# Performance work log

Measured on AMD Instinct MI355X. Metric: run time of the kernel, lower is better.

The kernel has to match this reference:

```python
import jax, jax.numpy as jnp
import numpy as np

NUM_HEADS = 16
NUM_KV_HEADS = 4
HEAD_DIM = 128
DIM = 2048
B, S = 2, 2048


def apply_rotary(t, cos, sin):
    # t: [B, S, H, D]; cos/sin: [S, D//2] -> broadcast [1, S, 1, D//2]
    tr = t.reshape(*t.shape[:-1], HEAD_DIM // 2, 2)
    t_r, t_i = tr[..., 0], tr[..., 1]
    c = cos[None, :, None, :]
    s = sin[None, :, None, :]
    o_r = t_r * c - t_i * s
    o_i = t_r * s + t_i * c
    return jnp.stack([o_r, o_i], axis=-1).reshape(t.shape)


def setup_inputs() -> dict:
    key = jax.random.key(0)
    ks = jax.random.split(key, 7)
    sc = 1.0 / np.sqrt(DIM)
    x = jax.random.normal(ks[0], (B, S, DIM), jnp.float32)
    pos = jnp.arange(S, dtype=jnp.float32)[:, None]
    inv_freq = 1.0 / (10000.0 ** (jnp.arange(0, HEAD_DIM, 2, dtype=jnp.float32) / HEAD_DIM))
    ang = pos * inv_freq[None, :]
    freqs_cos = jnp.cos(ang)
    freqs_sin = jnp.sin(ang)
    w_q = jax.random.normal(ks[1], (DIM, NUM_HEADS * HEAD_DIM), jnp.float32) * sc
    w_k = jax.random.normal(ks[2], (DIM, NUM_KV_HEADS * HEAD_DIM), jnp.float32) * sc
    w_v = jax.random.normal(ks[3], (DIM, NUM_KV_HEADS * HEAD_DIM), jnp.float32) * sc
    w_o = jax.random.normal(ks[4], (NUM_HEADS * HEAD_DIM, DIM), jnp.float32) * sc
    return {"x": x, "freqs_cos": freqs_cos, "freqs_sin": freqs_sin,
            "w_q": w_q, "w_k": w_k, "w_v": w_v, "w_o": w_o}


def reference(x, freqs_cos, freqs_sin, w_q, w_k, w_v, w_o):
    b, s, _ = x.shape
    kv_rep = NUM_HEADS // NUM_KV_HEADS
    q = (x @ w_q).reshape(b, s, NUM_HEADS, HEAD_DIM)
    k = (x @ w_k).reshape(b, s, NUM_KV_HEADS, HEAD_DIM)
    v = (x @ w_v).reshape(b, s, NUM_KV_HEADS, HEAD_DIM)
    q = apply_rotary(q, freqs_cos, freqs_sin)
    k = apply_rotary(k, freqs_cos, freqs_sin)
    # GQA: repeat KV heads to match query heads
    k = jnp.repeat(k, kv_rep, axis=2)
    v = jnp.repeat(v, kv_rep, axis=2)
    scores = jnp.einsum('bqhd,bkhd->bhqk', q, k) / np.sqrt(HEAD_DIM)
    causal = jnp.triu(jnp.full((s, s), -jnp.inf, jnp.float32), k=1)
    scores = scores + causal[None, None, :, :]
    attn = jax.nn.softmax(scores, axis=-1)
    out = jnp.einsum('bhqk,bkhd->bqhd', attn, v).reshape(b, s, NUM_HEADS * HEAD_DIM)
    return out @ w_o
```

## Files before the change

kernel.cpp:

```cpp
#include <hip/hip_runtime.h>
#include <stdint.h>

#define DIMSZ 2048
#define NH 16
#define NKV 4
#define HD 128
#define BATCH 2
#define SEQ 2048
#define MROWS (BATCH*SEQ)
#define NQKV (NH*HD + 2*NKV*HD)

typedef unsigned short u16;
typedef float f32x4 __attribute__((ext_vector_type(4)));
typedef short short8 __attribute__((ext_vector_type(8)));
typedef __bf16 bf16x8 __attribute__((ext_vector_type(8)));
typedef unsigned short u16x4 __attribute__((ext_vector_type(4)));

__device__ __forceinline__ u16 f2bf(float f) {
  __bf16 h = (__bf16)f;
  return __builtin_bit_cast(u16, h);
}

__device__ __forceinline__ float bf2f(u16 h) {
  union { uint32_t u; float f; } v; v.u = ((uint32_t)h) << 16; return v.f;
}

__device__ __forceinline__ void async16(void* lds, const void* g) {
  __builtin_amdgcn_global_load_lds(
      (const __attribute__((address_space(1))) void*)(g),
      (__attribute__((address_space(3))) void*)(lds), 16, 0, 0);
}

__device__ __forceinline__ bf16x8 load_frag(const u16* p) {
  short8 v = *reinterpret_cast<const short8*>(p);
  return __builtin_bit_cast(bf16x8, v);
}

__global__ void cast_x_kernel(const float* __restrict__ x, u16* __restrict__ xb) {
  int i = (blockIdx.x * blockDim.x + threadIdx.x) * 4;
  float4 v = *reinterpret_cast<const float4*>(x + i);
  u16x4 o;
  o.x = f2bf(v.x); o.y = f2bf(v.y); o.z = f2bf(v.z); o.w = f2bf(v.w);
  *reinterpret_cast<u16x4*>(xb + i) = o;
}

__global__ __launch_bounds__(1024) void wtrans_all_kernel(const float* __restrict__ wq,
                                                          const float* __restrict__ wk,
                                                          const float* __restrict__ wv,
                                                          const float* __restrict__ wo,
                                                          u16* __restrict__ wtqkv,
                                                          u16* __restrict__ wto) {
  __shared__ float t[32][33];
  int y = blockIdx.y;
  const float* src; int srcN; u16* dst; int nbase;
  if (y < 64)      { src = wq; srcN = 2048; dst = wtqkv;                          nbase = y * 32; }
  else if (y < 80) { src = wk; srcN = 512;  dst = wtqkv + (size_t)2048 * 2048;    nbase = (y - 64) * 32; }
  else if (y < 96) { src = wv; srcN = 512;  dst = wtqkv + (size_t)2560 * 2048;    nbase = (y - 80) * 32; }
  else             { src = wo; srcN = 2048; dst = wto;                            nbase = (y - 96) * 32; }
  int k0 = blockIdx.x * 32;
  int tx = threadIdx.x, ty = threadIdx.y;
  t[ty][tx] = src[(size_t)(k0 + ty) * srcN + nbase + tx];
  __syncthreads();
  dst[(size_t)(nbase + ty) * 2048 + k0 + tx] = f2bf(t[tx][ty]);
}

template <bool BF16OUT>
__global__ __launch_bounds__(256) void gemm_bt_kernel(const u16* __restrict__ A,
                                                      const u16* __restrict__ BT,
                                                      void* __restrict__ Cp,
                                                      int M, int N, int K, int gx) {
  __shared__ u16 As[128 * 64];
  __shared__ u16 Bs[128 * 64];
  const int tid = threadIdx.x;
  const int wave = tid >> 6, lane = tid & 63;
  const int l16 = lane & 15, lg = lane >> 4;
  const int nwg = gridDim.x;
  const int swz = (blockIdx.x & 7) * (nwg >> 3) + (blockIdx.x >> 3);
  const int bm = (swz / gx) * 128, bn = (swz % gx) * 128;
  const int wrow = (wave >> 1) * 64, wcol = (wave & 1) * 64;
  int srow[4], scol[4];
#pragma unroll
  for (int i = 0; i < 4; ++i) {
    int chunk = i * 4 + wave;
    srow[i] = chunk * 8 + (lane >> 3);
    scol[i] = ((lane & 7) ^ (srow[i] & 7)) * 8;
  }
  f32x4 acc[4][4] = {};
  for (int k0 = 0; k0 < K; k0 += 64) {
    __syncthreads();
#pragma unroll
    for (int i = 0; i < 4; ++i) {
      async16(&As[(i * 4 + wave) * 512], &A[(size_t)(bm + srow[i]) * K + k0 + scol[i]]);
      async16(&Bs[(i * 4 + wave) * 512], &BT[(size_t)(bn + srow[i]) * K + k0 + scol[i]]);
    }
    __syncthreads();
#pragma unroll
    for (int kk = 0; kk < 2; ++kk) {
      bf16x8 af[4], bfr[4];
#pragma unroll
      for (int mb = 0; mb < 4; ++mb) {
        int row = wrow + mb * 16 + l16;
        af[mb] = load_frag(&As[row * 64 + ((kk * 4 + lg) ^ (row & 7)) * 8]);
      }
#pragma unroll
      for (int nb = 0; nb < 4; ++nb) {
        int row = wcol + nb * 16 + l16;
        bfr[nb] = load_frag(&Bs[row * 64 + ((kk * 4 + lg) ^ (row & 7)) * 8]);
      }
#pragma unroll
      for (int mb = 0; mb < 4; ++mb)
#pragma unroll
        for (int nb = 0; nb < 4; ++nb)
          acc[mb][nb] = __builtin_amdgcn_mfma_f32_16x16x32_bf16(af[mb], bfr[nb], acc[mb][nb], 0, 0, 0);
    }
  }
#pragma unroll
  for (int mb = 0; mb < 4; ++mb)
#pragma unroll
    for (int nb = 0; nb < 4; ++nb)
#pragma unroll
      for (int r = 0; r < 4; ++r) {
        size_t idx = (size_t)(bm + wrow + mb * 16 + lg * 4 + r) * N + bn + wcol + nb * 16 + l16;
        if (BF16OUT) ((u16*)Cp)[idx] = f2bf(acc[mb][nb][r]);
        else         ((float*)Cp)[idx] = acc[mb][nb][r];
      }
}

__global__ void rope_k_kernel(const u16* __restrict__ qkv, const float* __restrict__ fc,
                              const float* __restrict__ fs, u16* __restrict__ Kb) {
  int gi = blockIdx.x * blockDim.x + threadIdx.x;
  int i = gi & 63;
  int t = gi >> 6;
  int s = t & (SEQ - 1), b = t >> 11;
  int kh = blockIdx.y;
  float c = fc[s * 64 + i], sn = fs[s * 64 + i];
  uint32_t pr = *reinterpret_cast<const uint32_t*>(&qkv[(size_t)t * NQKV + NH * HD + kh * HD + 2 * i]);
  float tr = bf2f((u16)(pr & 0xffff)), ti = bf2f((u16)(pr >> 16));
  uint32_t w = (uint32_t)f2bf(tr * c - ti * sn) |
               ((uint32_t)f2bf(tr * sn + ti * c) << 16);
  *reinterpret_cast<uint32_t*>(&Kb[((size_t)(b * NKV + kh) * SEQ + s) * HD + 2 * i]) = w;
}

__global__ __launch_bounds__(1024) void vtrans_kernel(const u16* __restrict__ qkv,
                                                      u16* __restrict__ vt) {
  __shared__ u16 t[32][33];
  int s0 = blockIdx.x * 32, d0 = blockIdx.y * 32;
  int bk = blockIdx.z;
  int b = bk >> 2, kh = bk & 3;
  int tx = threadIdx.x, ty = threadIdx.y;
  t[ty][tx] = qkv[(size_t)(b * SEQ + s0 + ty) * NQKV + NH * HD + NKV * HD + kh * HD + d0 + tx];
  __syncthreads();
  vt[((size_t)(b * NKV + kh) * HD + d0 + ty) * SEQ + s0 + tx] = t[tx][ty];
}

__global__ __launch_bounds__(256) void attn_kernel(const u16* __restrict__ qkv,
                                                   const float* __restrict__ fc,
                                                   const float* __restrict__ fs,
                                                   const u16* __restrict__ Kc,
                                                   const u16* __restrict__ VT,
                                                   u16* __restrict__ AO) {
  __shared__ u16 Ks[2][64 * 128];
  __shared__ u16 Vs[2][128 * 64];
  __shared__ u16 Ps[4][16 * 64];
  const int pairi = blockIdx.x;
  const int h = blockIdx.y, b = blockIdx.z;
  const int kvh = h >> 2;
  const int tid = threadIdx.x, wave = tid >> 6, lane = tid & 63;
  const int l16 = lane & 15, lg = lane >> 4;

  const u16* Kbase = Kc + (size_t)(b * NKV + kvh) * SEQ * HD;
  const u16* Vbase = VT + (size_t)(b * NKV + kvh) * HD * SEQ;

  bf16x8 onesf;
#pragma unroll
  for (int j = 0; j < 8; ++j) onesf[j] = __builtin_bit_cast(__bf16, (u16)0x3F80);

  int kOff[4], vOff[4], kDst[4], vDst[4];
#pragma unroll
  for (int i = 0; i < 4; ++i) {
    int chunk = i * 4 + wave;
    int krow = chunk * 4 + (lane >> 4);
    kOff[i] = krow * HD + ((lane & 15) ^ (krow & 15)) * 8;
    kDst[i] = chunk * 512;
    int vrow = chunk * 8 + (lane >> 3);
    vOff[i] = vrow * SEQ + ((lane & 7) ^ (vrow & 7)) * 8;
    vDst[i] = chunk * 512;
  }

  for (int sel = 0; sel < 2; ++sel) {
    const int qblk = sel ? pairi : (31 - pairi);
    const int qrow0 = qblk * 64 + wave * 16;
    const int rq = qrow0 + l16;

    const float qs = 0.12751689760098266f;
    const u16* Qrow = qkv + (size_t)(b * SEQ + rq) * NQKV + h * HD;
    const float* fcb = fc + (size_t)rq * 64;
    const float* fsb = fs + (size_t)rq * 64;
    bf16x8 qf[4];
#pragma unroll
    for (int c = 0; c < 4; ++c) {
      bf16x8 raw = load_frag(Qrow + c * 32 + lg * 8);
      float4 cc = *reinterpret_cast<const float4*>(fcb + c * 16 + lg * 4);
      float4 sv = *reinterpret_cast<const float4*>(fsb + c * 16 + lg * 4);
      bf16x8 q;
#pragma unroll
      for (int j = 0; j < 4; ++j) {
        float e = (float)raw[2 * j], od = (float)raw[2 * j + 1];
        float ce = (&cc.x)[j] * qs, se = (&sv.x)[j] * qs;
        q[2 * j]     = (__bf16)(e * ce - od * se);
        q[2 * j + 1] = (__bf16)(e * se + od * ce);
      }
      qf[c] = q;
    }

    f32x4 o[8] = {};
    f32x4 lsum = {};
    float m = -3e38f;

    __syncthreads();
#pragma unroll
    for (int i = 0; i < 4; ++i) {
      async16(&Ks[0][kDst[i]], Kbase + kOff[i]);
      async16(&Vs[0][vDst[i]], Vbase + vOff[i]);
    }

    for (int kt = 0; kt <= qblk; ++kt) {
      const int cur = kt & 1;
      __syncthreads();
      if (kt < qblk) {
        const int k0n = (kt + 1) * 64;
#pragma unroll
        for (int i = 0; i < 4; ++i) {
          async16(&Ks[cur ^ 1][kDst[i]], Kbase + (size_t)k0n * HD + kOff[i]);
          async16(&Vs[cur ^ 1][vDst[i]], Vbase + k0n + vOff[i]);
        }
      }

      f32x4 s[4] = {};
      __builtin_amdgcn_s_setprio(1);
#pragma unroll
      for (int cb = 0; cb < 4; ++cb) {
#pragma unroll
        for (int c = 0; c < 4; ++c) {
          bf16x8 kf = load_frag(&Ks[cur][(cb * 16 + l16) * 128 + (((c * 4 + lg) ^ l16) & 15) * 8]);
          s[cb] = __builtin_amdgcn_mfma_f32_16x16x32_bf16(kf, qf[c], s[cb], 0, 0, 0);
        }
      }
      __builtin_amdgcn_s_setprio(0);

      if (kt == qblk) {
        const int k0 = kt * 64;
#pragma unroll
        for (int cb = 0; cb < 4; ++cb) {
#pragma unroll
          for (int r = 0; r < 4; ++r) {
            int key = k0 + cb * 16 + lg * 4 + r;
            if (key > rq) s[cb][r] = -1e30f;
          }
        }
      }

      float v0 = fmaxf(fmaxf(fmaxf(s[0][0], s[0][1]), fmaxf(s[0][2], s[0][3])),
                       fmaxf(fmaxf(s[1][0], s[1][1]), fmaxf(s[1][2], s[1][3])));
      v0 = fmaxf(v0, fmaxf(fmaxf(fmaxf(s[2][0], s[2][1]), fmaxf(s[2][2], s[2][3])),
                           fmaxf(fmaxf(s[3][0], s[3][1]), fmaxf(s[3][2], s[3][3]))));
      v0 = fmaxf(v0, __shfl_xor(v0, 16));
      v0 = fmaxf(v0, __shfl_xor(v0, 32));

      bool need = v0 > m + 8.f;
      if (__any(need)) {
        float newm = fmaxf(m, v0);
        float sc = exp2f(m - newm);
        m = newm;
        float scR[4];
#pragma unroll
        for (int r = 0; r < 4; ++r) scR[r] = __shfl(sc, lg * 4 + r);
#pragma unroll
        for (int r = 0; r < 4; ++r) {
          lsum[r] *= scR[r];
#pragma unroll
          for (int db = 0; db < 8; ++db) o[db][r] *= scR[r];
        }
      }

#pragma unroll
      for (int cb = 0; cb < 4; ++cb) {
        uint32_t lo = (uint32_t)f2bf(exp2f(s[cb][0] - m)) |
                      ((uint32_t)f2bf(exp2f(s[cb][1] - m)) << 16);
        uint32_t hi = (uint32_t)f2bf(exp2f(s[cb][2] - m)) |
                      ((uint32_t)f2bf(exp2f(s[cb][3] - m)) << 16);
        int idx = (l16 * 64 + cb * 16 + lg * 4) ^ ((l16 & 7) << 3);
        uint64_t w = (uint64_t)lo | ((uint64_t)hi << 32);
        *reinterpret_cast<uint64_t*>(&Ps[wave][idx]) = w;
      }

      bf16x8 pf[2];
#pragma unroll
      for (int c = 0; c < 2; ++c)
        pf[c] = load_frag(&Ps[wave][(l16 * 64 + c * 32 + lg * 8) ^ ((l16 & 7) << 3)]);
      __builtin_amdgcn_s_setprio(1);
#pragma unroll
      for (int c = 0; c < 2; ++c)
        lsum = __builtin_amdgcn_mfma_f32_16x16x32_bf16(pf[c], onesf, lsum, 0, 0, 0);
#pragma unroll
      for (int db = 0; db < 8; ++db) {
#pragma unroll
        for (int c = 0; c < 2; ++c) {
          bf16x8 vf = load_frag(&Vs[cur][(db * 16 + l16) * 64 + ((c * 4 + lg) ^ (l16 & 7)) * 8]);
          o[db] = __builtin_amdgcn_mfma_f32_16x16x32_bf16(pf[c], vf, o[db], 0, 0, 0);
        }
      }
      __builtin_amdgcn_s_setprio(0);
    }

#pragma unroll
    for (int r = 0; r < 4; ++r) {
      float inv = 1.f / lsum[r];
      int rqo = qrow0 + lg * 4 + r;
      size_t dst = ((size_t)(b * SEQ + rqo) * NH + h) * HD;
#pragma unroll
      for (int db = 0; db < 8; ++db)
        AO[dst + db * 16 + l16] = f2bf(o[db][r] * inv);
    }
  }
}

extern "C" void kernel_launch(void* const* d_in, const int* in_sizes, int n_in,
                              void* d_out, int out_size, void* d_ws, size_t ws_size,
                              hipStream_t stream) {
  (void)in_sizes; (void)n_in; (void)out_size; (void)ws_size;
  const float* x  = (const float*)d_in[0];
  const float* fc = (const float*)d_in[1];
  const float* fs = (const float*)d_in[2];
  const float* wq = (const float*)d_in[3];
  const float* wk = (const float*)d_in[4];
  const float* wv = (const float*)d_in[5];
  const float* wo = (const float*)d_in[6];
  float* out = (float*)d_out;

  char* ws = (char*)d_ws;
  u16*  xb    = (u16*)(ws);
  u16*  wtqkv = (u16*)(ws + 16777216);
  u16*  wto   = (u16*)(ws + 29360128);
  u16*  qkv   = (u16*)(ws + 37748736);
  u16*  Kb    = (u16*)(ws + 62914560);
  u16*  VTb   = (u16*)(ws + 67108864);
  u16*  AOb   = (u16*)(ws + 71303168);

  cast_x_kernel<<<dim3(8192), dim3(256), 0, stream>>>(x, xb);
  wtrans_all_kernel<<<dim3(64, 160), dim3(32, 32), 0, stream>>>(wq, wk, wv, wo, wtqkv, wto);

  gemm_bt_kernel<true><<<dim3(768), dim3(256), 0, stream>>>(xb, wtqkv, qkv, MROWS, NQKV, DIMSZ, 24);

  rope_k_kernel<<<dim3(1024, 4), dim3(256), 0, stream>>>(qkv, fc, fs, Kb);
  vtrans_kernel<<<dim3(64, 4, 8), dim3(32, 32), 0, stream>>>(qkv, VTb);

  attn_kernel<<<dim3(16, 16, 2), dim3(256), 0, stream>>>(qkv, fc, fs, Kb, VTb, AOb);

  gemm_bt_kernel<false><<<dim3(512), dim3(256), 0, stream>>>(AOb, wto, out, MROWS, DIMSZ, DIMSZ, 16);
}
```

Before: 222.2 us.

## Use 256x256-tile 8-wave pipelined GEMM for the QKV projection

Adds a new GEMM kernel with 256x256 output tiles, 512 threads (8 waves) and double-buffered LDS. It issues async global-to-LDS loads in quarter stages interleaved with MFMA compute, uses s_setprio around the MFMA bursts and swizzles LDS to avoid bank conflicts. The QKV projection now runs on 192 workgroups instead of 768 128x128 tiles. The larger tiles raise arithmetic intensity and hide load latency, but 192 blocks underfill 256 CUs and register pressure is high.

```diff
diff --git a/kernel.cpp b/kernel.cpp
--- a/kernel.cpp
+++ b/kernel.cpp
@@ -64,6 +64,109 @@
   dst[(size_t)(nbase + ty) * 2048 + k0 + tx] = f2bf(t[tx][ty]);
 }
 
+#define COMPUTE_PAIR(q)                                                              \
+  {                                                                                  \
+    bf16x8 af[2][2];                                                                 \
+    _Pragma("unroll")                                                                \
+    for (int m2 = 0; m2 < 2; ++m2)                                                   \
+      _Pragma("unroll")                                                              \
+      for (int kk = 0; kk < 2; ++kk)                                                 \
+        af[m2][kk] = load_frag(&lds[buf][0][wm * 8192 +                              \
+            (((q) * 2 + m2) * 16 + l16) * 64 + ((kk * 4 + lg) ^ (l16 & 7)) * 8]);    \
+    __builtin_amdgcn_s_setprio(1);                                                   \
+    _Pragma("unroll")                                                                \
+    for (int m2 = 0; m2 < 2; ++m2)                                                   \
+      _Pragma("unroll")                                                              \
+      for (int ni = 0; ni < 4; ++ni)                                                 \
+        _Pragma("unroll")                                                            \
+        for (int kk = 0; kk < 2; ++kk)                                               \
+          acc[(q) * 2 + m2][ni] = __builtin_amdgcn_mfma_f32_16x16x32_bf16(           \
+              af[m2][kk], bper[ni][kk], acc[(q) * 2 + m2][ni], 0, 0, 0);             \
+    __builtin_amdgcn_s_setprio(0);                                                   \
+  }
+
+template <bool BF16OUT>
+__global__ __launch_bounds__(512, 2) void gemm8p_kernel(const u16* __restrict__ A,
+                                                        const u16* __restrict__ BT,
+                                                        void* __restrict__ Cp,
+                                                        int M, int N, int K, int gx) {
+  __shared__ u16 lds[2][2][16384];
+  const int tid = threadIdx.x;
+  const int wave = tid >> 6, lane = tid & 63;
+  const int l16 = lane & 15, lg = lane >> 4;
+  const int wm = wave >> 2, wn = wave & 3;
+  const int rloc = lane >> 3;
+  const int sOff = ((lane & 7) ^ rloc) * 8;
+  const int nwg = gridDim.x;
+  const int swz = (blockIdx.x & 7) * (nwg >> 3) + (blockIdx.x >> 3);
+  const int bm = (swz / gx) * 256, bn = (swz % gx) * 256;
+
+  f32x4 acc[8][4] = {};
+
+  auto stage = [&](int dstbuf, int x, int h, const u16* xp, int xr0, int kk0) {
+#pragma unroll
+    for (int j = 0; j < 2; ++j) {
+      int c = j * 8 + wave;
+      async16(&lds[dstbuf][x][h * 8192 + c * 512],
+              xp + (size_t)(xr0 + h * 128 + c * 8 + rloc) * K + kk0 + sOff);
+    }
+  };
+
+  stage(0, 0, 0, A, bm, 0);
+  stage(0, 0, 1, A, bm, 0);
+  stage(0, 1, 0, BT, bn, 0);
+  stage(0, 1, 1, BT, bn, 0);
+
+  const int NT = K >> 6;
+  for (int kt = 0; kt < NT; ++kt) {
+    const int buf = kt & 1, nbuf = buf ^ 1;
+    const int k0n = (kt + 1) << 6;
+    const bool pf = (kt + 1 < NT);
+    bf16x8 bper[4][2];
+
+    if (pf) {
+      stage(nbuf, 0, 0, A, bm, k0n);
+      asm volatile("s_waitcnt vmcnt(2)" ::: "memory");
+    } else {
+      asm volatile("s_waitcnt vmcnt(0)" ::: "memory");
+    }
+    __builtin_amdgcn_s_barrier();
+    __builtin_amdgcn_sched_barrier(0);
+#pragma unroll
+    for (int ni = 0; ni < 4; ++ni)
+#pragma unroll
+      for (int kk = 0; kk < 2; ++kk)
+        bper[ni][kk] = load_frag(&lds[buf][1][(wn >> 1) * 8192 +
+            ((wn & 1) * 64 + ni * 16 + l16) * 64 + ((kk * 4 + lg) ^ (l16 & 7)) * 8]);
+    COMPUTE_PAIR(0)
+    if (pf) stage(nbuf, 0, 1, A, bm, k0n);
+    __builtin_amdgcn_s_barrier();
+    __builtin_amdgcn_sched_barrier(0);
+    COMPUTE_PAIR(1)
+    if (pf) stage(nbuf, 1, 0, BT, bn, k0n);
+    __builtin_amdgcn_s_barrier();
+    __builtin_amdgcn_sched_barrier(0);
+    COMPUTE_PAIR(2)
+    if (pf) stage(nbuf, 1, 1, BT, bn, k0n);
+    __builtin_amdgcn_s_barrier();
+    __builtin_amdgcn_sched_barrier(0);
+    COMPUTE_PAIR(3)
+    __builtin_amdgcn_s_barrier();
+  }
+
+#pragma unroll
+  for (int mi = 0; mi < 8; ++mi)
+#pragma unroll
+    for (int ni = 0; ni < 4; ++ni)
+#pragma unroll
+      for (int r = 0; r < 4; ++r) {
+        size_t idx = (size_t)(bm + wm * 128 + mi * 16 + lg * 4 + r) * N +
+                     bn + wn * 64 + ni * 16 + l16;
+        if (BF16OUT) ((u16*)Cp)[idx] = f2bf(acc[mi][ni][r]);
+        else         ((float*)Cp)[idx] = acc[mi][ni][r];
+      }
+}
+
 template <bool BF16OUT>
 __global__ __launch_bounds__(256) void gemm_bt_kernel(const u16* __restrict__ A,
                                                       const u16* __restrict__ BT,
@@ -350,7 +453,7 @@
   cast_x_kernel<<<dim3(8192), dim3(256), 0, stream>>>(x, xb);
   wtrans_all_kernel<<<dim3(64, 160), dim3(32, 32), 0, stream>>>(wq, wk, wv, wo, wtqkv, wto);
 
-  gemm_bt_kernel<true><<<dim3(768), dim3(256), 0, stream>>>(xb, wtqkv, qkv, MROWS, NQKV, DIMSZ, 24);
+  gemm8p_kernel<true><<<dim3(192), dim3(512), 0, stream>>>(xb, wtqkv, qkv, MROWS, NQKV, DIMSZ, 12);
 
   rope_k_kernel<<<dim3(1024, 4), dim3(256), 0, stream>>>(qkv, fc, fs, Kb);
   vtrans_kernel<<<dim3(64, 4, 8), dim3(32, 32), 0, stream>>>(qkv, VTb);
```

New measurement: 211.7 us. 4.7% less time.
